# Kernel optimization log

Measured on AMD Instinct MI355X. Metric: run time of the kernel, lower is better.

Reference implementation:

```python
import jax, jax.numpy as jnp
import numpy as np

VOCAB, EMB, HID, LAYERS, SEQ, BATCH = 10000, 1024, 1024, 2, 64, 64


def setup_inputs() -> dict:
    key = jax.random.key(0)
    ks = jax.random.split(key, 12)
    b = 1.0 / np.sqrt(HID)
    u = lambda k, shape, bd: jax.random.uniform(k, shape, jnp.float32, -bd, bd)
    return {
        "inputs": jax.random.randint(ks[0], (SEQ, BATCH), 0, VOCAB),
        "hidden": jnp.zeros((LAYERS, BATCH, HID), jnp.float32),
        "emb": u(ks[1], (VOCAB, EMB), 0.1),
        "W0": u(ks[2], (EMB, 3 * HID), b),
        "U0": u(ks[3], (HID, 3 * HID), b),
        "bw0": u(ks[4], (3 * HID,), b),
        "bu0": u(ks[5], (3 * HID,), b),
        "W1": u(ks[6], (HID, 3 * HID), b),
        "U1": u(ks[7], (HID, 3 * HID), b),
        "bw1": u(ks[8], (3 * HID,), b),
        "bu1": u(ks[9], (3 * HID,), b),
        "fcW": u(ks[10], (VOCAB, HID), 0.1),
        "fcb": jnp.zeros((VOCAB,), jnp.float32),
    }


def gru_cell(x, h, W, U, bw, bu):
    gx = x @ W + bw            # [B, 3H]
    gh = h @ U + bu            # [B, 3H]
    i_r, i_z, i_n = jnp.split(gx, 3, axis=1)
    h_r, h_z, h_n = jnp.split(gh, 3, axis=1)
    r = jax.nn.sigmoid(i_r + h_r)
    z = jax.nn.sigmoid(i_z + h_z)
    h_tilde = jnp.tanh(i_n + r * h_n)
    return (1.0 - z) * h + z * h_tilde


def reference(inputs, hidden, emb, W0, U0, bw0, bu0, W1, U1, bw1, bu1, fcW, fcb):
    # dp_keep_prob = 1.0 -> dropout is identity (eval-mode reference)
    def step(hid, tok):
        x = emb[tok]                                   # [B, EMB]
        h0 = gru_cell(x, hid[0], W0, U0, bw0, bu0)     # [B, H]
        h1 = gru_cell(h0, hid[1], W1, U1, bw1, bu1)    # [B, H]
        y = h1 @ fcW.T + fcb                           # [B, V]
        return jnp.stack([h0, h1]), y

    hidden_f, logits = jax.lax.scan(step, hidden, inputs)
    return logits, hidden_f
```

## Files before the change

### kernel.cpp

```cpp
#include <hip/hip_runtime.h>
#include <math.h>

#define SEQL 64
#define BATCHN 64
#define HID 1024
#define EMBD 1024
#define VOCAB 10000
#define G3 3072
#define NPAD 10240
#define AROWS 4096
#define HSLOT 65536

typedef float f4v __attribute__((ext_vector_type(4)));
typedef unsigned short us4 __attribute__((ext_vector_type(4)));
typedef unsigned short us8 __attribute__((ext_vector_type(8)));
typedef __bf16 bf8v __attribute__((ext_vector_type(8)));

__device__ __forceinline__ unsigned short f2bf(float f) {
    unsigned u = __float_as_uint(f);
    u += 0x7fffu + ((u >> 16) & 1u);
    return (unsigned short)(u >> 16);
}
__device__ __forceinline__ float bf2f(unsigned short h) {
    return __uint_as_float(((unsigned)h) << 16);
}
__device__ __forceinline__ void split2(float f, unsigned short &hi, unsigned short &lo) {
    hi = f2bf(f);
    lo = f2bf(f - bf2f(hi));
}
__device__ __forceinline__ f4v mfma16(us8 a, us8 b, f4v c) {
    return __builtin_amdgcn_mfma_f32_16x16x32_bf16(
        __builtin_bit_cast(bf8v, a), __builtin_bit_cast(bf8v, b), c, 0, 0, 0);
}
__device__ __forceinline__ float sigmoidf_(float x) { return 1.f / (1.f + expf(-x)); }

__device__ __forceinline__ size_t htile_off(int b, int j) {
    return ((size_t)((((b >> 4) * 32 + (j >> 5)) * 64) + ((j >> 3) & 3) * 16 + (b & 15))) * 8 + (j & 7);
}

__global__ __launch_bounds__(256)
void tile_weights_kernel(const float* __restrict__ U0, const float* __restrict__ W1,
                         const float* __restrict__ U1, const float* __restrict__ W0,
                         unsigned short* __restrict__ hi, unsigned short* __restrict__ lo)
{
    __shared__ float tile[32][65];
    const int mat = blockIdx.z;
    const float* src = (mat == 0) ? U0 : (mat == 1) ? W1 : (mat == 2) ? U1 : W0;
    const int n0 = blockIdx.x * 64, k0 = blockIdx.y * 32;
    const int t = threadIdx.x, tx = t & 63, ty = t >> 6;
#pragma unroll
    for (int s = 0; s < 8; s++)
        tile[ty * 8 + s][tx] = src[(size_t)(k0 + ty * 8 + s) * G3 + n0 + tx];
    __syncthreads();
    const int c = t >> 6, lane = t & 63, fr = lane & 15, kg = lane >> 4;
    const int cc = (n0 >> 4) + c;
    const size_t off = (((size_t)(mat * 192 + cc) * 32 + (k0 >> 5)) * 64 + lane) * 8;
    us8 h8, l8;
#pragma unroll
    for (int e = 0; e < 8; e++) {
        unsigned short a, b;
        split2(tile[kg * 8 + e][c * 16 + fr], a, b);
        h8[e] = a; l8[e] = b;
    }
    *(us8*)(hi + off) = h8;
    *(us8*)(lo + off) = l8;
}

__global__ void fc_pad_split_kernel(const float* __restrict__ fcW,
                                    unsigned short* __restrict__ hi, unsigned short* __restrict__ lo)
{
    size_t i = ((size_t)blockIdx.x * 256 + threadIdx.x) * 4;
    size_t row = i >> 10;
    f4v v = {0.f, 0.f, 0.f, 0.f};
    if (row < VOCAB) v = *(const f4v*)(fcW + i);
    us4 h, l;
#pragma unroll
    for (int j = 0; j < 4; j++) { unsigned short a, b; split2(v[j], a, b); h[j] = a; l[j] = b; }
    *(us4*)(hi + i) = h;
    *(us4*)(lo + i) = l;
}

__global__ void fcb_pad_kernel(const float* __restrict__ fcb, float* __restrict__ fcb_pad)
{
    int idx = blockIdx.x * 256 + threadIdx.x;
    if (idx < NPAD) fcb_pad[idx] = (idx < VOCAB) ? fcb[idx] : 0.f;
}

__global__ void small_prep_kernel(const float* __restrict__ hidden,
                                  unsigned short* __restrict__ h0th, unsigned short* __restrict__ h0tl,
                                  unsigned short* __restrict__ h1th, unsigned short* __restrict__ h1tl)
{
    int idx = blockIdx.x * 256 + threadIdx.x;
    if (idx < BATCHN * HID) {
        int b = idx >> 10, j = idx & 1023;
        size_t o = htile_off(b, j);
        unsigned short a1, b1;
        split2(hidden[idx], a1, b1);                 h0th[o] = a1; h0tl[o] = b1;
        split2(hidden[BATCHN * HID + idx], a1, b1);  h1th[o] = a1; h1tl[o] = b1;
    }
}

__global__ __launch_bounds__(256)
void gx0_gemm_kernel(const int* __restrict__ tok, const float* __restrict__ emb,
                     const unsigned short* __restrict__ Wthi, const unsigned short* __restrict__ Wtlo,
                     float* __restrict__ C)
{
    __shared__ unsigned short Ah[128][40], Al[128][40];
    const int bswz = blockIdx.x;
    const int xcd = bswz & 7, s = bswz >> 3;
    const int col0 = (xcd + 8 * (s >> 5)) * 128;
    const int row0 = (s & 31) * 128;
    const int tid = threadIdx.x;
    const int lane = tid & 63, wave = tid >> 6;
    const int wm = wave >> 1, wn = wave & 1;
    const int srow = tid >> 1;
    const int shalf = (tid & 1) * 16;

    const float* asrc = emb + (size_t)tok[row0 + srow] * EMBD + shalf;
    const int fr = lane & 15, fk = (lane >> 4) * 8;
    const int cc0 = (col0 >> 4) + wn * 4;

    f4v a[4];
#pragma unroll
    for (int q = 0; q < 4; q++) a[q] = *(const f4v*)(asrc + q * 4);

    f4v acc[4][4] = {};
    for (int k0 = 0; k0 < EMBD; k0 += 32) {
        __syncthreads();
        us8 ahv[2], alv[2];
#pragma unroll
        for (int q = 0; q < 4; q++)
#pragma unroll
            for (int j = 0; j < 4; j++) {
                unsigned short h, l;
                split2(a[q][j], h, l);
                ahv[q >> 1][(q & 1) * 4 + j] = h;
                alv[q >> 1][(q & 1) * 4 + j] = l;
            }
        *(us8*)(&Ah[srow][shalf]) = ahv[0];     *(us8*)(&Ah[srow][shalf + 8]) = ahv[1];
        *(us8*)(&Al[srow][shalf]) = alv[0];     *(us8*)(&Al[srow][shalf + 8]) = alv[1];
        __syncthreads();
        if (k0 + 32 < EMBD) {
#pragma unroll
            for (int q = 0; q < 4; q++) a[q] = *(const f4v*)(asrc + k0 + 32 + q * 4);
        }
        const int ks = k0 >> 5;
        us8 bfh[4], bfl[4];
#pragma unroll
        for (int n = 0; n < 4; n++) {
            const size_t bo = (((size_t)(3 * 192 + cc0 + n) * 32 + ks) * 64 + lane) * 8;
            bfh[n] = *(const us8*)(Wthi + bo);
            bfl[n] = *(const us8*)(Wtlo + bo);
        }
        us8 afh[4], afl[4];
#pragma unroll
        for (int m = 0; m < 4; m++) {
            afh[m] = *(const us8*)(&Ah[wm * 64 + m * 16 + fr][fk]);
            afl[m] = *(const us8*)(&Al[wm * 64 + m * 16 + fr][fk]);
        }
#pragma unroll
        for (int n = 0; n < 4; n++)
#pragma unroll
            for (int m = 0; m < 4; m++) {
                acc[m][n] = mfma16(afh[m], bfh[n], acc[m][n]);
                acc[m][n] = mfma16(afh[m], bfl[n], acc[m][n]);
                acc[m][n] = mfma16(afl[m], bfh[n], acc[m][n]);
            }
    }
    const int fq = lane >> 4;
#pragma unroll
    for (int m = 0; m < 4; m++)
#pragma unroll
        for (int n = 0; n < 4; n++)
#pragma unroll
            for (int i = 0; i < 4; i++) {
                int r = row0 + wm * 64 + m * 16 + fq * 4 + i;
                int c = col0 + wn * 64 + n * 16 + fr;
                C[(size_t)r * G3 + c] = acc[m][n][i];
            }
}

__global__ __launch_bounds__(256)
void logits_gemm_kernel(const unsigned short* __restrict__ h1t_hi, const unsigned short* __restrict__ h1t_lo,
                        const unsigned short* __restrict__ Bhi, const unsigned short* __restrict__ Blo,
                        const float* __restrict__ bias, float* __restrict__ C)
{
    __shared__ unsigned short Bh[128][40], Bl[128][40];
    const int bswz = blockIdx.x;
    const int xcd = bswz & 7, s = bswz >> 3;
    const int col0 = (xcd + 8 * (s >> 5)) * 128;
    const int row0 = (s & 31) * 128;
    const int t0 = row0 >> 6;
    const int tid = threadIdx.x;
    const int lane = tid & 63, wave = tid >> 6;
    const int wm = wave >> 1, wn = wave & 1;
    const int srow = tid >> 1;
    const int shalf = (tid & 1) * 16;

    const unsigned short* bh_src = Bhi + (size_t)(col0 + srow) * HID + shalf;
    const unsigned short* bl_src = Blo + (size_t)(col0 + srow) * HID + shalf;

    f4v acc[4][4] = {};
    us8 bh2[2], bl2[2];
    bh2[0] = *(const us8*)(bh_src);  bh2[1] = *(const us8*)(bh_src + 8);
    bl2[0] = *(const us8*)(bl_src);  bl2[1] = *(const us8*)(bl_src + 8);

    const int fr = lane & 15, fk = (lane >> 4) * 8;
    const size_t abase = ((size_t)(t0 + wm) * 128) * 512 + (size_t)lane * 8;

    for (int k0 = 0; k0 < HID; k0 += 32) {
        __syncthreads();
        *(us8*)(&Bh[srow][shalf]) = bh2[0];  *(us8*)(&Bh[srow][shalf + 8]) = bh2[1];
        *(us8*)(&Bl[srow][shalf]) = bl2[0];  *(us8*)(&Bl[srow][shalf + 8]) = bl2[1];
        __syncthreads();
        if (k0 + 32 < HID) {
            bh2[0] = *(const us8*)(bh_src + k0 + 32);  bh2[1] = *(const us8*)(bh_src + k0 + 40);
            bl2[0] = *(const us8*)(bl_src + k0 + 32);  bl2[1] = *(const us8*)(bl_src + k0 + 40);
        }
        const int ks = k0 >> 5;
        us8 afh[4], afl[4];
#pragma unroll
        for (int m = 0; m < 4; m++) {
            const size_t ao = abase + (size_t)(m * 32 + ks) * 512;
            afh[m] = *(const us8*)(h1t_hi + ao);
            afl[m] = *(const us8*)(h1t_lo + ao);
        }
#pragma unroll
        for (int n = 0; n < 4; n++) {
            us8 bfh = *(const us8*)(&Bh[wn * 64 + n * 16 + fr][fk]);
            us8 bfl = *(const us8*)(&Bl[wn * 64 + n * 16 + fr][fk]);
#pragma unroll
            for (int m = 0; m < 4; m++) {
                acc[m][n] = mfma16(afh[m], bfh, acc[m][n]);
                acc[m][n] = mfma16(afh[m], bfl, acc[m][n]);
                acc[m][n] = mfma16(afl[m], bfh, acc[m][n]);
            }
        }
    }
    const int fq = lane >> 4;
#pragma unroll
    for (int m = 0; m < 4; m++)
#pragma unroll
        for (int n = 0; n < 4; n++)
#pragma unroll
            for (int i = 0; i < 4; i++) {
                int r = row0 + wm * 64 + m * 16 + fq * 4 + i;
                int c = col0 + wn * 64 + n * 16 + fr;
                float v = acc[m][n][i] + bias[c];
                if (c < VOCAB) C[(size_t)r * VOCAB + c] = v;
            }
}

template <int T0, int T1>
__global__ __launch_bounds__(512, 1)
void step_gemm_kernel(const unsigned short* __restrict__ h0hi, const unsigned short* __restrict__ h0lo,
                      const unsigned short* __restrict__ h1hi, const unsigned short* __restrict__ h1lo,
                      const unsigned short* __restrict__ Wthi, const unsigned short* __restrict__ Wtlo,
                      float* __restrict__ P)
{
    const int tid = threadIdx.x, lane = tid & 63, wave = tid >> 6;
    const int jc = blockIdx.x >> 2, kq = blockIdx.x & 3;
    const int ks = kq * 8 + wave;
    const size_t abase = ((size_t)ks * 64 + lane) * 8;

    f4v acc[9][4] = {};
    us8 ah[4], al[4];

    if (T0 < 6) {
#pragma unroll
        for (int m = 0; m < 4; m++) {
            ah[m] = *(const us8*)(h0hi + abase + (size_t)m * 16384);
            al[m] = *(const us8*)(h0lo + abase + (size_t)m * 16384);
        }
#pragma unroll
        for (int t2 = T0; t2 < ((T1 < 6) ? T1 : 6); ++t2) {
            const int mat = t2 / 3, g = t2 % 3;
            const size_t base = (((size_t)(mat * 192 + g * 64 + jc) * 32 + ks) * 64 + lane) * 8;
            us8 bh = *(const us8*)(Wthi + base);
            us8 bl = *(const us8*)(Wtlo + base);
#pragma unroll
            for (int m = 0; m < 4; ++m) {
                acc[t2][m] = mfma16(ah[m], bh, acc[t2][m]);
                acc[t2][m] = mfma16(ah[m], bl, acc[t2][m]);
                acc[t2][m] = mfma16(al[m], bh, acc[t2][m]);
            }
        }
    }
    if (T1 > 6) {
#pragma unroll
        for (int m = 0; m < 4; m++) {
            ah[m] = *(const us8*)(h1hi + abase + (size_t)m * 16384);
            al[m] = *(const us8*)(h1lo + abase + (size_t)m * 16384);
        }
#pragma unroll
        for (int t2 = 6; t2 < T1; ++t2) {
            const int g = t2 % 3;
            const size_t base = (((size_t)(2 * 192 + g * 64 + jc) * 32 + ks) * 64 + lane) * 8;
            us8 bh = *(const us8*)(Wthi + base);
            us8 bl = *(const us8*)(Wtlo + base);
#pragma unroll
            for (int m = 0; m < 4; ++m) {
                acc[t2][m] = mfma16(ah[m], bh, acc[t2][m]);
                acc[t2][m] = mfma16(ah[m], bl, acc[t2][m]);
                acc[t2][m] = mfma16(al[m], bh, acc[t2][m]);
            }
        }
    }

    __shared__ f4v red[4][3][4][64];
    const int c0lo = T0 / 3, c0hi = (T1 + 2) / 3;
#pragma unroll
    for (int stride = 4; stride >= 1; stride >>= 1) {
#pragma unroll
        for (int c = c0lo; c < c0hi; ++c) {
            if (wave >= stride && wave < 2 * stride) {
#pragma unroll
                for (int u = 0; u < 3; ++u) {
                    const int t2 = c * 3 + u;
                    if (t2 >= T0 && t2 < T1) {
#pragma unroll
                        for (int m = 0; m < 4; ++m)
                            red[wave - stride][u][m][lane] = acc[t2][m];
                    }
                }
            }
            __syncthreads();
            if (wave < stride) {
#pragma unroll
                for (int u = 0; u < 3; ++u) {
                    const int t2 = c * 3 + u;
                    if (t2 >= T0 && t2 < T1) {
#pragma unroll
                        for (int m = 0; m < 4; ++m)
                            acc[t2][m] += red[wave][u][m][lane];
                    }
                }
            }
            __syncthreads();
        }
    }

    if (wave == 0) {
        const int rrow = (lane >> 4) * 4, rcol = lane & 15;
#pragma unroll
        for (int t2 = T0; t2 < T1; ++t2)
#pragma unroll
            for (int m = 0; m < 4; ++m)
#pragma unroll
                for (int i = 0; i < 4; ++i)
                    P[(((size_t)kq * 9 + t2) * 64 + (m * 16 + rrow + i)) * 1024 + jc * 16 + rcol]
                        = acc[t2][m][i];
    }
}

template <int T0, int T1>
__global__ __launch_bounds__(256)
void step_reduce_kernel(const float* __restrict__ P, const float* __restrict__ gx0next,
                        const float* __restrict__ bw0, const float* __restrict__ bu0,
                        const float* __restrict__ bw1, const float* __restrict__ bu1,
                        const unsigned short* __restrict__ h0hi, const unsigned short* __restrict__ h0lo,
                        const unsigned short* __restrict__ h1hi, const unsigned short* __restrict__ h1lo,
                        unsigned short* __restrict__ h0o_hi, unsigned short* __restrict__ h0o_lo,
                        unsigned short* __restrict__ h1o_hi, unsigned short* __restrict__ h1o_lo)
{
    const int idx = blockIdx.x * 256 + threadIdx.x;
    const int b = idx >> 10, j = idx & 1023;
    float G[9];
#pragma unroll
    for (int t2 = T0; t2 < T1; t2++) {
        const float* p = P + ((size_t)t2 * 64 + b) * 1024 + j;
        G[t2] = (p[0] + p[(size_t)9 * 64 * 1024])
              + (p[(size_t)18 * 64 * 1024] + p[(size_t)27 * 64 * 1024]);
    }
    const size_t po = htile_off(b, j);
    if (T0 == 0) {
        float sr  = gx0next[(size_t)b * G3 + j]            + bw0[j]           + G[0] + bu0[j];
        float sz  = gx0next[(size_t)b * G3 + HID + j]      + bw0[HID + j]     + G[1] + bu0[HID + j];
        float gxn = gx0next[(size_t)b * G3 + 2 * HID + j]  + bw0[2 * HID + j];
        float ghn = G[2] + bu0[2 * HID + j];
        float r = sigmoidf_(sr);
        float z = sigmoidf_(sz);
        float ht = tanhf(gxn + r * ghn);
        float hp = bf2f(h0hi[po]) + bf2f(h0lo[po]);
        float hn = (1.f - z) * hp + z * ht;
        unsigned short hh, hl2; split2(hn, hh, hl2);
        h0o_hi[po] = hh; h0o_lo[po] = hl2;
    }
    if (T1 > 3) {
        float sr  = G[3] + bw1[j]           + G[6] + bu1[j];
        float sz  = G[4] + bw1[HID + j]     + G[7] + bu1[HID + j];
        float gxn = G[5] + bw1[2 * HID + j];
        float ghn = G[8] + bu1[2 * HID + j];
        float r = sigmoidf_(sr);
        float z = sigmoidf_(sz);
        float ht = tanhf(gxn + r * ghn);
        float hp = bf2f(h1hi[po]) + bf2f(h1lo[po]);
        float hn = (1.f - z) * hp + z * ht;
        unsigned short hh, hl2; split2(hn, hh, hl2);
        h1o_hi[po] = hh; h1o_lo[po] = hl2;
    }
}

__global__ void hidden_out_kernel(const unsigned short* __restrict__ h0hi, const unsigned short* __restrict__ h0lo,
                                  const unsigned short* __restrict__ h1hi, const unsigned short* __restrict__ h1lo,
                                  float* __restrict__ out)
{
    int i = blockIdx.x * 256 + threadIdx.x;
    if (i < BATCHN * HID) {
        int b = i >> 10, j = i & 1023;
        size_t o = htile_off(b, j);
        out[i] = bf2f(h0hi[o]) + bf2f(h0lo[o]);
        out[BATCHN * HID + i] = bf2f(h1hi[o]) + bf2f(h1lo[o]);
    }
}

extern "C" void kernel_launch(void* const* d_in, const int* in_sizes, int n_in,
                              void* d_out, int out_size, void* d_ws, size_t ws_size,
                              hipStream_t stream)
{
    (void)in_sizes; (void)n_in; (void)out_size;
    const int*   tok    = (const int*)  d_in[0];
    const float* hidden = (const float*)d_in[1];
    const float* emb    = (const float*)d_in[2];
    const float* W0     = (const float*)d_in[3];
    const float* U0     = (const float*)d_in[4];
    const float* bw0    = (const float*)d_in[5];
    const float* bu0    = (const float*)d_in[6];
    const float* W1     = (const float*)d_in[7];
    const float* U1     = (const float*)d_in[8];
    const float* bw1    = (const float*)d_in[9];
    const float* bu1    = (const float*)d_in[10];
    const float* fcW    = (const float*)d_in[11];
    const float* fcb    = (const float*)d_in[12];
    float* out = (float*)d_out;

    char* wsp = (char*)d_ws;
    size_t used = 0;
    auto alloc = [&](size_t bytes) -> char* {
        char* p = wsp + used;
        used += (bytes + 255) & ~(size_t)255;
        return p;
    };
    unsigned short* Wt_hi = (unsigned short*)alloc((size_t)4 * G3 * HID * 2);
    unsigned short* Wt_lo = (unsigned short*)alloc((size_t)4 * G3 * HID * 2);
    float*          GX0   = (float*)alloc((size_t)AROWS * G3 * 4);
    unsigned short* H0Thi = (unsigned short*)alloc((size_t)SEQL * HSLOT * 2);
    unsigned short* H0Tlo = (unsigned short*)alloc((size_t)SEQL * HSLOT * 2);
    unsigned short* H1Thi = (unsigned short*)alloc((size_t)SEQL * HSLOT * 2);
    unsigned short* H1Tlo = (unsigned short*)alloc((size_t)SEQL * HSLOT * 2);
    float*          P0    = (float*)alloc((size_t)4 * 9 * BATCHN * HID * 4);
    float*          P1    = (float*)alloc((size_t)4 * 9 * BATCHN * HID * 4);
    unsigned short* h0ith = (unsigned short*)alloc((size_t)HSLOT * 2);
    unsigned short* h0itl = (unsigned short*)alloc((size_t)HSLOT * 2);
    unsigned short* h1ith = (unsigned short*)alloc((size_t)HSLOT * 2);
    unsigned short* h1itl = (unsigned short*)alloc((size_t)HSLOT * 2);
    if (used > ws_size) return;

    unsigned short* fcWhi = Wt_hi;
    unsigned short* fcWlo = Wt_lo;
    float*          fcbp  = (float*)((char*)Wt_hi + (size_t)NPAD * HID * 2);

    tile_weights_kernel<<<dim3(48, 32, 4), 256, 0, stream>>>(U0, W1, U1, W0, Wt_hi, Wt_lo);
    small_prep_kernel<<<256, 256, 0, stream>>>(hidden, h0ith, h0itl, h1ith, h1itl);
    gx0_gemm_kernel<<<768, 256, 0, stream>>>(tok, emb, Wt_hi, Wt_lo, GX0);

    step_gemm_kernel<0, 3><<<256, 512, 0, stream>>>(
        h0ith, h0itl, h1ith, h1itl, Wt_hi, Wt_lo, P0);
    step_reduce_kernel<0, 3><<<256, 256, 0, stream>>>(
        P0, GX0, bw0, bu0, bw1, bu1,
        h0ith, h0itl, h1ith, h1itl,
        H0Thi, H0Tlo,
        H1Thi + (size_t)63 * HSLOT, H1Tlo + (size_t)63 * HSLOT);

    for (int t = 0; t < 63; t++) {
        const unsigned short* h0h = H0Thi + (size_t)t * HSLOT;
        const unsigned short* h0l = H0Tlo + (size_t)t * HSLOT;
        const unsigned short* a1h = (t == 0) ? h1ith : H1Thi + (size_t)(t - 1) * HSLOT;
        const unsigned short* a1l = (t == 0) ? h1itl : H1Tlo + (size_t)(t - 1) * HSLOT;
        float* Pb = ((t & 1) == 0) ? P1 : P0;
        step_gemm_kernel<0, 9><<<256, 512, 0, stream>>>(
            h0h, h0l, a1h, a1l, Wt_hi, Wt_lo, Pb);
        step_reduce_kernel<0, 9><<<256, 256, 0, stream>>>(
            Pb, GX0 + (size_t)(t + 1) * BATCHN * G3, bw0, bu0, bw1, bu1,
            h0h, h0l, a1h, a1l,
            H0Thi + (size_t)(t + 1) * HSLOT, H0Tlo + (size_t)(t + 1) * HSLOT,
            H1Thi + (size_t)t * HSLOT, H1Tlo + (size_t)t * HSLOT);
    }
    step_gemm_kernel<3, 9><<<256, 512, 0, stream>>>(
        H0Thi + (size_t)63 * HSLOT, H0Tlo + (size_t)63 * HSLOT,
        H1Thi + (size_t)62 * HSLOT, H1Tlo + (size_t)62 * HSLOT,
        Wt_hi, Wt_lo, P0);
    step_reduce_kernel<3, 9><<<256, 256, 0, stream>>>(
        P0, GX0, bw0, bu0, bw1, bu1,
        H0Thi + (size_t)63 * HSLOT, H0Tlo + (size_t)63 * HSLOT,
        H1Thi + (size_t)62 * HSLOT, H1Tlo + (size_t)62 * HSLOT,
        h0ith, h0itl,
        H1Thi + (size_t)63 * HSLOT, H1Tlo + (size_t)63 * HSLOT);

    hidden_out_kernel<<<256, 256, 0, stream>>>(
        H0Thi + (size_t)63 * HSLOT, H0Tlo + (size_t)63 * HSLOT,
        H1Thi + (size_t)63 * HSLOT, H1Tlo + (size_t)63 * HSLOT,
        out + (size_t)AROWS * VOCAB);

    fc_pad_split_kernel<<<NPAD, 256, 0, stream>>>(fcW, fcWhi, fcWlo);
    fcb_pad_kernel<<<(NPAD + 255) / 256, 256, 0, stream>>>(fcb, fcbp);
    logits_gemm_kernel<<<2560, 256, 0, stream>>>(
        H1Thi, H1Tlo, fcWhi, fcWlo, fcbp, out);
}
```

Measured before the change: 1.556 ms.

## Pre-tile fc weights for direct MFMA loads and split step GEMM K across 8 blocks

The fc weight matrix is now converted straight into the MFMA fragment layout, so the logits GEMM loads B fragments from global memory and no longer stages them through LDS with barriers. Separately, the per-step recurrent GEMM goes from 256 blocks of 512 threads to 512 blocks of 256 threads, splitting K into 8 slices instead of 4. Each block does a simpler single-round LDS reduction, and the reduce kernel now sums 8 partials. This trades more partial-sum traffic for better occupancy and shorter reductions on the serial critical path. The double-buffered P arrays become a single buffer.

```diff
diff --git a/kernel.cpp b/kernel.cpp
--- a/kernel.cpp
+++ b/kernel.cpp
@@ -66,18 +66,37 @@
     *(us8*)(lo + off) = l8;
 }
 
-__global__ void fc_pad_split_kernel(const float* __restrict__ fcW,
-                                    unsigned short* __restrict__ hi, unsigned short* __restrict__ lo)
-{
-    size_t i = ((size_t)blockIdx.x * 256 + threadIdx.x) * 4;
-    size_t row = i >> 10;
-    f4v v = {0.f, 0.f, 0.f, 0.f};
-    if (row < VOCAB) v = *(const f4v*)(fcW + i);
-    us4 h, l;
-#pragma unroll
-    for (int j = 0; j < 4; j++) { unsigned short a, b; split2(v[j], a, b); h[j] = a; l[j] = b; }
-    *(us4*)(hi + i) = h;
-    *(us4*)(lo + i) = l;
+__global__ __launch_bounds__(256)
+void tile_fc_kernel(const float* __restrict__ fcW,
+                    unsigned short* __restrict__ hi, unsigned short* __restrict__ lo)
+{
+    const int cc = blockIdx.x;
+    const int tid = threadIdx.x;
+#pragma unroll
+    for (int q = 0; q < 8; q++) {
+        const int o = tid * 8 + q;
+        const int ks = o >> 6, lane = o & 63;
+        const int fr = lane & 15, kg = lane >> 4;
+        const int row = cc * 16 + fr;
+        const int col = ks * 32 + kg * 8;
+        us8 h8, l8;
+        if (row < VOCAB) {
+            f4v v0 = *(const f4v*)(fcW + (size_t)row * HID + col);
+            f4v v1 = *(const f4v*)(fcW + (size_t)row * HID + col + 4);
+#pragma unroll
+            for (int e = 0; e < 4; e++) {
+                unsigned short a, b;
+                split2(v0[e], a, b); h8[e] = a; l8[e] = b;
+                split2(v1[e], a, b); h8[4 + e] = a; l8[4 + e] = b;
+            }
+        } else {
+            h8 = (us8){0,0,0,0,0,0,0,0};
+            l8 = (us8){0,0,0,0,0,0,0,0};
+        }
+        const size_t off = (((size_t)cc * 32 + ks) * 64 + lane) * 8;
+        *(us8*)(hi + off) = h8;
+        *(us8*)(lo + off) = l8;
+    }
 }
 
 __global__ void fcb_pad_kernel(const float* __restrict__ fcb, float* __restrict__ fcb_pad)
@@ -185,7 +204,6 @@
                         const unsigned short* __restrict__ Bhi, const unsigned short* __restrict__ Blo,
                         const float* __restrict__ bias, float* __restrict__ C)
 {
-    __shared__ unsigned short Bh[128][40], Bl[128][40];
     const int bswz = blockIdx.x;
     const int xcd = bswz & 7, s = bswz >> 3;
     const int col0 = (xcd + 8 * (s >> 5)) * 128;
@@ -194,31 +212,14 @@
     const int tid = threadIdx.x;
     const int lane = tid & 63, wave = tid >> 6;
     const int wm = wave >> 1, wn = wave & 1;
-    const int srow = tid >> 1;
-    const int shalf = (tid & 1) * 16;
-
-    const unsigned short* bh_src = Bhi + (size_t)(col0 + srow) * HID + shalf;
-    const unsigned short* bl_src = Blo + (size_t)(col0 + srow) * HID + shalf;
+    const int fr = lane & 15;
+    const int cc0 = (col0 >> 4) + wn * 4;
 
     f4v acc[4][4] = {};
-    us8 bh2[2], bl2[2];
-    bh2[0] = *(const us8*)(bh_src);  bh2[1] = *(const us8*)(bh_src + 8);
-    bl2[0] = *(const us8*)(bl_src);  bl2[1] = *(const us8*)(bl_src + 8);
-
-    const int fr = lane & 15, fk = (lane >> 4) * 8;
     const size_t abase = ((size_t)(t0 + wm) * 128) * 512 + (size_t)lane * 8;
 
-    for (int k0 = 0; k0 < HID; k0 += 32) {
-        __syncthreads();
-        *(us8*)(&Bh[srow][shalf]) = bh2[0];  *(us8*)(&Bh[srow][shalf + 8]) = bh2[1];
-        *(us8*)(&Bl[srow][shalf]) = bl2[0];  *(us8*)(&Bl[srow][shalf + 8]) = bl2[1];
-        __syncthreads();
-        if (k0 + 32 < HID) {
-            bh2[0] = *(const us8*)(bh_src + k0 + 32);  bh2[1] = *(const us8*)(bh_src + k0 + 40);
-            bl2[0] = *(const us8*)(bl_src + k0 + 32);  bl2[1] = *(const us8*)(bl_src + k0 + 40);
-        }
-        const int ks = k0 >> 5;
-        us8 afh[4], afl[4];
+    for (int ks = 0; ks < 32; ks++) {
+        us8 afh[4], afl[4], bfh[4], bfl[4];
 #pragma unroll
         for (int m = 0; m < 4; m++) {
             const size_t ao = abase + (size_t)(m * 32 + ks) * 512;
@@ -227,15 +228,18 @@
         }
 #pragma unroll
         for (int n = 0; n < 4; n++) {
-            us8 bfh = *(const us8*)(&Bh[wn * 64 + n * 16 + fr][fk]);
-            us8 bfl = *(const us8*)(&Bl[wn * 64 + n * 16 + fr][fk]);
+            const size_t bo = (((size_t)(cc0 + n) * 32 + ks) * 64 + lane) * 8;
+            bfh[n] = *(const us8*)(Bhi + bo);
+            bfl[n] = *(const us8*)(Blo + bo);
+        }
+#pragma unroll
+        for (int n = 0; n < 4; n++)
 #pragma unroll
             for (int m = 0; m < 4; m++) {
-                acc[m][n] = mfma16(afh[m], bfh, acc[m][n]);
-                acc[m][n] = mfma16(afh[m], bfl, acc[m][n]);
-                acc[m][n] = mfma16(afl[m], bfh, acc[m][n]);
-            }
-        }
+                acc[m][n] = mfma16(afh[m], bfh[n], acc[m][n]);
+                acc[m][n] = mfma16(afh[m], bfl[n], acc[m][n]);
+                acc[m][n] = mfma16(afl[m], bfh[n], acc[m][n]);
+            }
     }
     const int fq = lane >> 4;
 #pragma unroll
@@ -252,15 +256,15 @@
 }
 
 template <int T0, int T1>
-__global__ __launch_bounds__(512, 1)
+__global__ __launch_bounds__(256)
 void step_gemm_kernel(const unsigned short* __restrict__ h0hi, const unsigned short* __restrict__ h0lo,
                       const unsigned short* __restrict__ h1hi, const unsigned short* __restrict__ h1lo,
                       const unsigned short* __restrict__ Wthi, const unsigned short* __restrict__ Wtlo,
                       float* __restrict__ P)
 {
     const int tid = threadIdx.x, lane = tid & 63, wave = tid >> 6;
-    const int jc = blockIdx.x >> 2, kq = blockIdx.x & 3;
-    const int ks = kq * 8 + wave;
+    const int jc = blockIdx.x >> 3, kh = blockIdx.x & 7;
+    const int ks = kh * 4 + wave;
     const size_t abase = ((size_t)ks * 64 + lane) * 8;
 
     f4v acc[9][4] = {};
@@ -307,49 +311,38 @@
         }
     }
 
-    __shared__ f4v red[4][3][4][64];
-    const int c0lo = T0 / 3, c0hi = (T1 + 2) / 3;
-#pragma unroll
-    for (int stride = 4; stride >= 1; stride >>= 1) {
-#pragma unroll
-        for (int c = c0lo; c < c0hi; ++c) {
-            if (wave >= stride && wave < 2 * stride) {
-#pragma unroll
-                for (int u = 0; u < 3; ++u) {
-                    const int t2 = c * 3 + u;
-                    if (t2 >= T0 && t2 < T1) {
-#pragma unroll
-                        for (int m = 0; m < 4; ++m)
-                            red[wave - stride][u][m][lane] = acc[t2][m];
-                    }
+    __shared__ f4v red[4][2][4][64];
+    const int rrow = (lane >> 4) * 4, rcol = lane & 15;
+#pragma unroll
+    for (int c = 0; c < 5; ++c) {
+        const int ta = 2 * c, tb = 2 * c + 1;
+        if (tb >= T0 && ta < T1) {
+#pragma unroll
+            for (int u = 0; u < 2; ++u) {
+                const int t2 = 2 * c + u;
+                if (t2 >= T0 && t2 < T1) {
+#pragma unroll
+                    for (int m = 0; m < 4; ++m)
+                        red[wave][u][m][lane] = acc[t2][m];
                 }
             }
             __syncthreads();
-            if (wave < stride) {
-#pragma unroll
-                for (int u = 0; u < 3; ++u) {
-                    const int t2 = c * 3 + u;
-                    if (t2 >= T0 && t2 < T1) {
-#pragma unroll
-                        for (int m = 0; m < 4; ++m)
-                            acc[t2][m] += red[wave][u][m][lane];
-                    }
+#pragma unroll
+            for (int s2 = 0; s2 < 2; ++s2) {
+                const int combo = wave * 2 + s2;
+                const int u = combo >> 2, m = combo & 3;
+                const int t2 = 2 * c + u;
+                if (t2 >= T0 && t2 < T1) {
+                    f4v v = (red[0][u][m][lane] + red[1][u][m][lane])
+                          + (red[2][u][m][lane] + red[3][u][m][lane]);
+#pragma unroll
+                    for (int i = 0; i < 4; ++i)
+                        P[(((size_t)kh * 9 + t2) * 64 + (m * 16 + rrow + i)) * 1024 + jc * 16 + rcol]
+                            = v[i];
                 }
             }
             __syncthreads();
         }
-    }
-
-    if (wave == 0) {
-        const int rrow = (lane >> 4) * 4, rcol = lane & 15;
-#pragma unroll
-        for (int t2 = T0; t2 < T1; ++t2)
-#pragma unroll
-            for (int m = 0; m < 4; ++m)
-#pragma unroll
-                for (int i = 0; i < 4; ++i)
-                    P[(((size_t)kq * 9 + t2) * 64 + (m * 16 + rrow + i)) * 1024 + jc * 16 + rcol]
-                        = acc[t2][m][i];
     }
 }
 
@@ -369,8 +362,13 @@
 #pragma unroll
     for (int t2 = T0; t2 < T1; t2++) {
         const float* p = P + ((size_t)t2 * 64 + b) * 1024 + j;
-        G[t2] = (p[0] + p[(size_t)9 * 64 * 1024])
-              + (p[(size_t)18 * 64 * 1024] + p[(size_t)27 * 64 * 1024]);
+        float s0 = 0.f, s1 = 0.f;
+#pragma unroll
+        for (int kh = 0; kh < 4; kh++) {
+            s0 += p[(size_t)(kh * 9) * 64 * 1024];
+            s1 += p[(size_t)((kh + 4) * 9) * 64 * 1024];
+        }
+        G[t2] = s0 + s1;
     }
     const size_t po = htile_off(b, j);
     if (T0 == 0) {
@@ -448,8 +446,7 @@
     unsigned short* H0Tlo = (unsigned short*)alloc((size_t)SEQL * HSLOT * 2);
     unsigned short* H1Thi = (unsigned short*)alloc((size_t)SEQL * HSLOT * 2);
     unsigned short* H1Tlo = (unsigned short*)alloc((size_t)SEQL * HSLOT * 2);
-    float*          P0    = (float*)alloc((size_t)4 * 9 * BATCHN * HID * 4);
-    float*          P1    = (float*)alloc((size_t)4 * 9 * BATCHN * HID * 4);
+    float*          P     = (float*)alloc((size_t)8 * 9 * BATCHN * HID * 4);
     unsigned short* h0ith = (unsigned short*)alloc((size_t)HSLOT * 2);
     unsigned short* h0itl = (unsigned short*)alloc((size_t)HSLOT * 2);
     unsigned short* h1ith = (unsigned short*)alloc((size_t)HSLOT * 2);
@@ -464,10 +461,10 @@
     small_prep_kernel<<<256, 256, 0, stream>>>(hidden, h0ith, h0itl, h1ith, h1itl);
     gx0_gemm_kernel<<<768, 256, 0, stream>>>(tok, emb, Wt_hi, Wt_lo, GX0);
 
-    step_gemm_kernel<0, 3><<<256, 512, 0, stream>>>(
-        h0ith, h0itl, h1ith, h1itl, Wt_hi, Wt_lo, P0);
+    step_gemm_kernel<0, 3><<<512, 256, 0, stream>>>(
+        h0ith, h0itl, h1ith, h1itl, Wt_hi, Wt_lo, P);
     step_reduce_kernel<0, 3><<<256, 256, 0, stream>>>(
-        P0, GX0, bw0, bu0, bw1, bu1,
+        P, GX0, bw0, bu0, bw1, bu1,
         h0ith, h0itl, h1ith, h1itl,
         H0Thi, H0Tlo,
         H1Thi + (size_t)63 * HSLOT, H1Tlo + (size_t)63 * HSLOT);
@@ -477,21 +474,20 @@
         const unsigned short* h0l = H0Tlo + (size_t)t * HSLOT;
         const unsigned short* a1h = (t == 0) ? h1ith : H1Thi + (size_t)(t - 1) * HSLOT;
         const unsigned short* a1l = (t == 0) ? h1itl : H1Tlo + (size_t)(t - 1) * HSLOT;
-        float* Pb = ((t & 1) == 0) ? P1 : P0;
-        step_gemm_kernel<0, 9><<<256, 512, 0, stream>>>(
-            h0h, h0l, a1h, a1l, Wt_hi, Wt_lo, Pb);
+        step_gemm_kernel<0, 9><<<512, 256, 0, stream>>>(
+            h0h, h0l, a1h, a1l, Wt_hi, Wt_lo, P);
         step_reduce_kernel<0, 9><<<256, 256, 0, stream>>>(
-            Pb, GX0 + (size_t)(t + 1) * BATCHN * G3, bw0, bu0, bw1, bu1,
+            P, GX0 + (size_t)(t + 1) * BATCHN * G3, bw0, bu0, bw1, bu1,
             h0h, h0l, a1h, a1l,
             H0Thi + (size_t)(t + 1) * HSLOT, H0Tlo + (size_t)(t + 1) * HSLOT,
             H1Thi + (size_t)t * HSLOT, H1Tlo + (size_t)t * HSLOT);
     }
-    step_gemm_kernel<3, 9><<<256, 512, 0, stream>>>(
+    step_gemm_kernel<3, 9><<<512, 256, 0, stream>>>(
         H0Thi + (size_t)63 * HSLOT, H0Tlo + (size_t)63 * HSLOT,
         H1Thi + (size_t)62 * HSLOT, H1Tlo + (size_t)62 * HSLOT,
-        Wt_hi, Wt_lo, P0);
+        Wt_hi, Wt_lo, P);
     step_reduce_kernel<3, 9><<<256, 256, 0, stream>>>(
-        P0, GX0, bw0, bu0, bw1, bu1,
+        P, GX0, bw0, bu0, bw1, bu1,
         H0Thi + (size_t)63 * HSLOT, H0Tlo + (size_t)63 * HSLOT,
         H1Thi + (size_t)62 * HSLOT, H1Tlo + (size_t)62 * HSLOT,
         h0ith, h0itl,
@@ -502,7 +498,7 @@
         H1Thi + (size_t)63 * HSLOT, H1Tlo + (size_t)63 * HSLOT,
         out + (size_t)AROWS * VOCAB);
 
-    fc_pad_split_kernel<<<NPAD, 256, 0, stream>>>(fcW, fcWhi, fcWlo);
+    tile_fc_kernel<<<NPAD / 16, 256, 0, stream>>>(fcW, fcWhi, fcWlo);
     fcb_pad_kernel<<<(NPAD + 255) / 256, 256, 0, stream>>>(fcb, fcbp);
     logits_gemm_kernel<<<2560, 256, 0, stream>>>(
         H1Thi, H1Tlo, fcWhi, fcWlo, fcbp, out);
```

Result: no change. 1.555 ms (-0.1%).
